# Kernel optimization log

Measured on AMD Instinct MI355X. Metric: run time of the kernel, lower is better.

The kernel has to match this reference:

```python
import jax, jax.numpy as jnp
import numpy as np

TIME_GAP_BUCKETS = 64
B, L, H, MAX_T = 256, 200, 256, 256
VOCAB, N_GROUPS = 50000, 16
EPS = 1e-5


def setup_inputs() -> dict:
    key = jax.random.key(0)
    ks = jax.random.split(key, 16)
    lengths = jax.random.randint(ks[0], (B,), 0, L + 1)
    mask = jnp.arange(L)[None, :] < lengths[:, None]

    def toks(k, hi):  # jagged padded-dense: zeros past each row's length
        return jnp.where(mask, jax.random.randint(k, (B, L), 0, hi), 0)

    inp = {
        'history_tokens': toks(ks[1], VOCAB),
        'history_post_tokens': toks(ks[2], VOCAB),
        'history_author_tokens': toks(ks[3], VOCAB),
        'history_action_tokens': toks(ks[4], VOCAB),
        'history_time_gap': toks(ks[5], TIME_GAP_BUCKETS + 1),
        'history_group_ids': jnp.where(mask, jnp.sort(jax.random.randint(ks[6], (B, L), 1, N_GROUPS + 1), axis=1), 0),
        'lengths': lengths,
    }
    s = 0.02
    inp['token_emb'] = jax.random.normal(ks[7], (VOCAB, H)) * s
    inp['ln_gamma'] = jnp.ones((6 * H,))
    inp['ln_beta'] = jnp.zeros((6 * H,))
    inp['w1'] = jax.random.normal(ks[8], (6 * H, 4 * H)) * (1.0 / np.sqrt(6 * H)).astype(np.float32)
    inp['b1'] = jnp.zeros((4 * H,))
    inp['w2'] = jax.random.normal(ks[9], (4 * H, H)) * (1.0 / np.sqrt(4 * H)).astype(np.float32)
    inp['b2'] = jnp.zeros((H,))
    inp['time_gap_emb'] = (jax.random.normal(ks[10], (TIME_GAP_BUCKETS + 1, H)) * s).at[0].set(0.0)  # padding_idx=0
    inp['group_emb'] = (jax.random.normal(ks[11], (N_GROUPS + 1, H)) * s).at[0].set(0.0)  # padding_idx=0
    inp['pos_emb'] = jax.random.normal(ks[12], (MAX_T, H)) * s
    inp['sep_token'] = jax.random.normal(ks[13], (H,)) * 0.02
    return inp


def _layernorm(x, g, b):
    mu = jnp.mean(x, axis=-1, keepdims=True)
    var = jnp.mean(jnp.square(x - mu), axis=-1, keepdims=True)
    return (x - mu) * jax.lax.rsqrt(var + EPS) * g + b


def _merge_with_sep(event_tokens, group_ids, mask, sep_token):
    # mask is a prefix mask (positions < lengths), so valid tokens are contiguous.
    Bn, Ln, Hn = event_tokens.shape
    next_mask = jnp.pad(mask[:, 1:], ((0, 0), (0, 1)))
    next_group = jnp.pad(group_ids[:, 1:], ((0, 0), (0, 1)))
    sep_after = mask & next_mask & (group_ids != next_group)  # insert sep after token i
    seps_before = jnp.cumsum(sep_after, axis=1) - sep_after.astype(jnp.int32)  # exclusive scan
    token_pos = jnp.arange(Ln)[None, :] + seps_before  # position within merged piece list
    total = mask.sum(axis=1) + sep_after.sum(axis=1)  # [B] merged piece count
    offset = MAX_T - total  # right-align; negative -> leading pieces dropped
    tok_idx = offset[:, None] + token_pos
    sep_idx = tok_idx + 1
    tok_idx = jnp.where(mask & (tok_idx >= 0), tok_idx, MAX_T)  # MAX_T => dropped
    sep_idx = jnp.where(sep_after & (sep_idx >= 0), sep_idx, MAX_T)
    sep_rows = jnp.broadcast_to(sep_token, (Ln, Hn))

    def scatter_one(ev, ti, si):
        buf = jnp.zeros((MAX_T, Hn), ev.dtype)
        buf = buf.at[ti].set(ev, mode='drop')
        buf = buf.at[si].set(sep_rows, mode='drop')
        return buf

    merged = jax.vmap(scatter_one)(event_tokens, tok_idx, sep_idx)
    merged_len = jnp.minimum(total, MAX_T)
    merged_mask = jnp.arange(MAX_T)[None, :] >= (MAX_T - merged_len)[:, None]
    return merged, merged_mask


def reference(history_tokens, history_post_tokens, history_author_tokens,
              history_action_tokens, history_time_gap, history_group_ids,
              lengths, token_emb, ln_gamma, ln_beta, w1, b1, w2, b2,
              time_gap_emb, group_emb, pos_emb, sep_token):
    mask = jnp.arange(L)[None, :] < lengths[:, None]
    hh = token_emb[history_tokens]
    ph = token_emb[history_post_tokens]
    ah = token_emb[history_author_tokens]
    ch = token_emb[history_action_tokens]
    th = time_gap_emb[jnp.clip(history_time_gap, 0, TIME_GAP_BUCKETS)]
    gh = group_emb[history_group_ids]
    ev = jnp.concatenate([hh, ph, ah, ch, th, gh], axis=-1)  # [B, L, 6H]
    x = _layernorm(ev, ln_gamma, ln_beta)
    x = jax.nn.silu(x @ w1 + b1)  # dropout is identity in eval mode
    event_tokens = x @ w2 + b2  # [B, L, H]
    merged, mm = _merge_with_sep(event_tokens, history_group_ids, mask, sep_token)
    merged = (merged + pos_emb[None]) * mm[..., None].astype(merged.dtype)
    return merged, mm
```

## Files before the change

### kernel.cpp

```cpp
#include <hip/hip_runtime.h>
#include <hip/hip_bf16.h>
#include <math.h>

#define B_    256
#define L_    200
#define H_    256
#define MAXT  256
#define SIXH  1536
#define FOURH 1024
#define NPOS  (B_ * L_)

typedef __attribute__((ext_vector_type(8))) short short8;
typedef __attribute__((ext_vector_type(4))) float f32x4;

typedef __attribute__((address_space(3))) void lds_void;
typedef const __attribute__((address_space(1))) void gbl_void;

#define ASM_BAR() asm volatile("s_barrier" ::: "memory")
#define VMCNT4()  asm volatile("s_waitcnt vmcnt(4)" ::: "memory")
#define VMCNT0()  asm volatile("s_waitcnt vmcnt(0)" ::: "memory")

__global__ void scan_offsets(const int* __restrict__ lengths,
                             int* __restrict__ offsets) {
  if (threadIdx.x == 0) {
    int acc = 0;
    for (int b = 0; b < B_; b++) { offsets[b] = acc; acc += lengths[b]; }
    offsets[B_] = acc;
  }
}

__global__ void zero_pad_x(__hip_bfloat16* __restrict__ x,
                           const int* __restrict__ offsets) {
  int total = offsets[B_];
  int padded = (total + 255) & ~255;
  int row = total + blockIdx.x;
  if (row >= padded) return;
  int t = threadIdx.x;
#pragma unroll
  for (int j = 0; j < 6; j++)
    x[(size_t)row * SIXH + j * 256 + t] = __float2bfloat16(0.0f);
}

__global__ void tpos_kernel(const int* __restrict__ gids,
                            const int* __restrict__ lengths,
                            const int* __restrict__ offsets,
                            int* __restrict__ tpos) {
  int b = blockIdx.x, t = threadIdx.x;
  __shared__ int g[L_];
  int len = lengths[b];
  for (int l = t; l < len; l += 64) g[l] = gids[b * L_ + l];
  __syncthreads();
  if (t != 0) return;
  int base = offsets[b];
  int nsep = 0;
  for (int l = 0; l + 1 < len; l++)
    if (g[l] != g[l + 1]) nsep++;
  int total = len + nsep;
  int off = MAXT - total;
  int sb = 0;
  for (int l = 0; l < len; l++) {
    int ti = off + l + sb;
    tpos[base + l] = (ti >= 0) ? (b * MAXT + ti) : -1;
    if (l + 1 < len && g[l] != g[l + 1]) sb++;
  }
}

__global__ void transpose_to_bf16(const float* __restrict__ in,
                                  __hip_bfloat16* __restrict__ out,
                                  int R, int C) {
  __shared__ float tile[32][33];
  int tc = blockIdx.x, tr = blockIdx.y;
  int tx = threadIdx.x & 31, ty = threadIdx.x >> 5;
#pragma unroll
  for (int i = 0; i < 4; i++) {
    int r = tr * 32 + ty + i * 8;
    int c = tc * 32 + tx;
    tile[ty + i * 8][tx] = in[(size_t)r * C + c];
  }
  __syncthreads();
#pragma unroll
  for (int i = 0; i < 4; i++) {
    int orow = tc * 32 + ty + i * 8;
    int ocol = tr * 32 + tx;
    out[(size_t)orow * R + ocol] = __float2bfloat16(tile[tx][ty + i * 8]);
  }
}

__global__ void embed_ln_kernel(const int* __restrict__ tok0,
                                const int* __restrict__ tok1,
                                const int* __restrict__ tok2,
                                const int* __restrict__ tok3,
                                const int* __restrict__ tgap,
                                const int* __restrict__ gid,
                                const int* __restrict__ lengths,
                                const int* __restrict__ offsets,
                                const float* __restrict__ token_emb,
                                const float* __restrict__ tg_emb,
                                const float* __restrict__ g_emb,
                                const float* __restrict__ gamma,
                                const float* __restrict__ beta,
                                __hip_bfloat16* __restrict__ xout) {
  int l = blockIdx.x, b = blockIdx.y;
  if (l >= lengths[b]) return;
  int pos = b * L_ + l;
  int row = offsets[b] + l;
  int t = threadIdx.x;
  int wv = t >> 6;
  int ln = t & 63;
  int c4 = ln * 4;

  const float* tab;
  int idx;
  if (wv == 0)      { tab = token_emb; idx = tok0[pos]; }
  else if (wv == 1) { tab = token_emb; idx = tok1[pos]; }
  else if (wv == 2) { tab = token_emb; idx = tok2[pos]; }
  else if (wv == 3) { tab = token_emb; idx = tok3[pos]; }
  else if (wv == 4) { tab = tg_emb;    idx = min(max(tgap[pos], 0), 64); }
  else              { tab = g_emb;     idx = gid[pos]; }

  float4 v = *(const float4*)&tab[(size_t)idx * H_ + c4];

  float s = v.x + v.y + v.z + v.w;
  float q = v.x * v.x + v.y * v.y + v.z * v.z + v.w * v.w;
#pragma unroll
  for (int o = 32; o; o >>= 1) { s += __shfl_down(s, o); q += __shfl_down(q, o); }
  __shared__ float ps[6], pq[6];
  if (ln == 0) { ps[wv] = s; pq[wv] = q; }
  __syncthreads();
  float ts = 0.f, tq = 0.f;
#pragma unroll
  for (int k = 0; k < 6; k++) { ts += ps[k]; tq += pq[k]; }
  float mu = ts * (1.0f / 1536.0f);
  float var = tq * (1.0f / 1536.0f) - mu * mu;
  float rstd = rsqrtf(var + 1e-5f);

  int cbase = wv * 256 + c4;
  float4 gm = *(const float4*)&gamma[cbase];
  float4 bt = *(const float4*)&beta[cbase];
  float y0 = (v.x - mu) * rstd * gm.x + bt.x;
  float y1 = (v.y - mu) * rstd * gm.y + bt.y;
  float y2 = (v.z - mu) * rstd * gm.z + bt.z;
  float y3 = (v.w - mu) * rstd * gm.w + bt.w;
  __hip_bfloat16 h0 = __float2bfloat16(y0), h1 = __float2bfloat16(y1);
  __hip_bfloat16 h2 = __float2bfloat16(y2), h3 = __float2bfloat16(y3);
  ushort4 pk;
  pk.x = *(unsigned short*)&h0; pk.y = *(unsigned short*)&h1;
  pk.z = *(unsigned short*)&h2; pk.w = *(unsigned short*)&h3;
  *(ushort4*)&xout[(size_t)row * SIXH + cbase] = pk;
}

__global__ __launch_bounds__(512, 2)
void gemm1_8ph(const __hip_bfloat16* __restrict__ A,
               const __hip_bfloat16* __restrict__ Bt,
               const float* __restrict__ bias,
               __hip_bfloat16* __restrict__ out,
               const int* __restrict__ total_ptr) {
  constexpr int K = SIXH;
  constexpr int NT = K / 64;
  constexpr int N = FOURH;

  extern __shared__ __align__(16) char lds[];

  int total = total_ptr[0];
  int padded = (total + 255) & ~255;
  int num_mt = padded >> 8;

  int bid = blockIdx.x;
  int xcd = bid & 7;
  int slot = bid >> 3;
  int nt = slot & 3;
  int mtb = slot >> 2;
  int n0 = nt * 256;

  int tid = threadIdx.x;
  int lane = tid & 63;
  int w = tid >> 6;
  int wave_m = w >> 2;
  int wave_n = w & 3;

  int r15 = lane & 15, g = lane >> 4;
  int slot_r = (((r15 & 1) << 2) | g) ^ (r15 >> 1);
  int lane_off = (r15 >> 1) * 128 + slot_r * 16;

  int s0 = (tid & 7) ^ ((tid >> 3) & 7);
  int scol = (s0 & 3) * 8;
  int row0 = ((tid >> 3) << 1) + (s0 >> 2);
  int ldst0 = w * 1024;

  float bv4[4];
#pragma unroll
  for (int ni = 0; ni < 4; ni++)
    bv4[ni] = bias[n0 + wave_n * 64 + ni * 16 + r15];

#define REGA(d, h) (lds + (d) * 65536 + (h) * 16384)
#define REGB(d, h) (lds + (d) * 65536 + 32768 + (h) * 16384)

#define STAGE(P, t0, kt, h, rb)                                                \
  do {                                                                         \
    __builtin_amdgcn_global_load_lds(                                          \
        (gbl_void*)((P) + (size_t)((t0) + row0) * K + (kt) * 64 + (h) * 32 +   \
                    scol),                                                     \
        (lds_void*)((rb) + ldst0), 16, 0, 0);                                  \
    __builtin_amdgcn_global_load_lds(                                          \
        (gbl_void*)((P) + (size_t)((t0) + row0 + 128) * K + (kt) * 64 +        \
                    (h) * 32 + scol),                                          \
        (lds_void*)((rb) + 8192 + ldst0), 16, 0, 0);                           \
  } while (0)

  for (int mt = xcd + 8 * mtb; mt < num_mt; mt += 64) {
    int m0 = mt * 256;

    f32x4 acc[8][4] = {};

    STAGE(A, m0, 0, 0, REGA(0, 0));
    STAGE(Bt, n0, 0, 0, REGB(0, 0));
    STAGE(A, m0, 0, 1, REGA(0, 1));
    STAGE(Bt, n0, 0, 1, REGB(0, 1));
    STAGE(A, m0, 1, 0, REGA(1, 0));
    STAGE(Bt, n0, 1, 0, REGB(1, 0));
    VMCNT4();
    ASM_BAR();

    for (int kt = 0; kt < NT; ++kt) {
      int d = kt & 1;
      int kc1 = (kt + 1 < NT) ? kt + 1 : NT - 1;
      int kc2 = (kt + 2 < NT) ? kt + 2 : NT - 1;
      char* A0 = REGA(d, 0); char* A1 = REGA(d, 1);
      char* B0 = REGB(d, 0); char* B1 = REGB(d, 1);
      char* An1 = REGA(d ^ 1, 1);
      char* Bn1 = REGB(d ^ 1, 1);

      short8 a[4], b[4];

#pragma unroll
      for (int ni = 0; ni < 4; ni++)
        b[ni] = *(const short8*)(B0 + (wave_n * 64 + ni * 16) * 64 + lane_off);
#pragma unroll
      for (int j = 0; j < 4; j++)
        a[j] = *(const short8*)(A0 + (wave_m * 128 + j * 16) * 64 + lane_off);
      STAGE(A, m0, kc1, 1, An1);
      __builtin_amdgcn_s_setprio(1);
#pragma unroll
      for (int j = 0; j < 4; j++)
#pragma unroll
        for (int ni = 0; ni < 4; ni++)
          acc[j][ni] = __builtin_amdgcn_mfma_f32_16x16x32_bf16(a[j], b[ni],
                                                               acc[j][ni], 0, 0, 0);
      __builtin_amdgcn_s_setprio(0);
#pragma unroll
      for (int j = 0; j < 4; j++)
        a[j] = *(const short8*)(A0 + (wave_m * 128 + (4 + j) * 16) * 64 + lane_off);
      STAGE(Bt, n0, kc1, 1, Bn1);
      __builtin_amdgcn_s_setprio(1);
#pragma unroll
      for (int j = 0; j < 4; j++)
#pragma unroll
        for (int ni = 0; ni < 4; ni++)
          acc[4 + j][ni] = __builtin_amdgcn_mfma_f32_16x16x32_bf16(
              a[j], b[ni], acc[4 + j][ni], 0, 0, 0);
      __builtin_amdgcn_s_setprio(0);
      ASM_BAR();

#pragma unroll
      for (int ni = 0; ni < 4; ni++)
        b[ni] = *(const short8*)(B1 + (wave_n * 64 + ni * 16) * 64 + lane_off);
#pragma unroll
      for (int j = 0; j < 4; j++)
        a[j] = *(const short8*)(A1 + (wave_m * 128 + j * 16) * 64 + lane_off);
      STAGE(A, m0, kc2, 0, A0);
      __builtin_amdgcn_s_setprio(1);
#pragma unroll
      for (int j = 0; j < 4; j++)
#pragma unroll
        for (int ni = 0; ni < 4; ni++)
          acc[j][ni] = __builtin_amdgcn_mfma_f32_16x16x32_bf16(a[j], b[ni],
                                                               acc[j][ni], 0, 0, 0);
      __builtin_amdgcn_s_setprio(0);
#pragma unroll
      for (int j = 0; j < 4; j++)
        a[j] = *(const short8*)(A1 + (wave_m * 128 + (4 + j) * 16) * 64 + lane_off);
      STAGE(Bt, n0, kc2, 0, B0);
      __builtin_amdgcn_s_setprio(1);
#pragma unroll
      for (int j = 0; j < 4; j++)
#pragma unroll
        for (int ni = 0; ni < 4; ni++)
          acc[4 + j][ni] = __builtin_amdgcn_mfma_f32_16x16x32_bf16(
              a[j], b[ni], acc[4 + j][ni], 0, 0, 0);
      __builtin_amdgcn_s_setprio(0);
      VMCNT4();
      ASM_BAR();
    }
    VMCNT0();

    int r0 = g * 4;
#pragma unroll
    for (int mi = 0; mi < 8; mi++)
#pragma unroll
      for (int ni = 0; ni < 4; ni++) {
        int col = n0 + wave_n * 64 + ni * 16 + r15;
        float bv = bv4[ni];
#pragma unroll
        for (int r = 0; r < 4; r++) {
          int row = m0 + wave_m * 128 + mi * 16 + r0 + r;
          float v = acc[mi][ni][r] + bv;
          v = v / (1.0f + __expf(-v));
          out[(size_t)row * N + col] = __float2bfloat16(v);
        }
      }
  }
#undef STAGE
#undef REGA
#undef REGB
}

__global__ void gemm2_scatter(const __hip_bfloat16* __restrict__ A,
                              const __hip_bfloat16* __restrict__ Bt,
                              const float* __restrict__ bias,
                              const int* __restrict__ tpos,
                              const float* __restrict__ pos_emb,
                              float* __restrict__ out,
                              const int* __restrict__ total_ptr,
                              int N, int K) {
  int m0 = blockIdx.y * 128;
  int total = total_ptr[0];
  int padded = (total + 127) & ~127;
  if (m0 >= padded) return;

  __shared__ __hip_bfloat16 As[128 * 64];
  __shared__ __hip_bfloat16 Bs[128 * 64];
  int n0 = blockIdx.x * 128;
  int tid = threadIdx.x;
  int lane = tid & 63, wid = tid >> 6;
  int wm = (wid >> 1) * 64, wn = (wid & 1) * 64;

  int srow = (lane >> 3);
  int scol = (lane & 7) * 8;

  f32x4 acc[4][4] = {};

  for (int k0 = 0; k0 < K; k0 += 64) {
#pragma unroll
    for (int i = 0; i < 4; i++) {
      int c = wid * 4 + i;
      int row = c * 8 + srow;
      __builtin_amdgcn_global_load_lds(
          (gbl_void*)&A[(size_t)(m0 + row) * K + k0 + scol],
          (lds_void*)(As + c * 512), 16, 0, 0);
      __builtin_amdgcn_global_load_lds(
          (gbl_void*)&Bt[(size_t)(n0 + row) * K + k0 + scol],
          (lds_void*)(Bs + c * 512), 16, 0, 0);
    }
    __syncthreads();
#pragma unroll
    for (int kk = 0; kk < 64; kk += 32) {
      short8 a[4], bb[4];
#pragma unroll
      for (int m = 0; m < 4; m++)
        a[m] = *(const short8*)&As[(wm + m * 16 + (lane & 15)) * 64 + kk +
                                   8 * (lane >> 4)];
#pragma unroll
      for (int n = 0; n < 4; n++)
        bb[n] = *(const short8*)&Bs[(wn + n * 16 + (lane & 15)) * 64 + kk +
                                    8 * (lane >> 4)];
#pragma unroll
      for (int m = 0; m < 4; m++)
#pragma unroll
        for (int n = 0; n < 4; n++)
          acc[m][n] = __builtin_amdgcn_mfma_f32_16x16x32_bf16(a[m], bb[n],
                                                              acc[m][n], 0, 0, 0);
    }
    __syncthreads();
  }

  int r0 = (lane >> 4) * 4;
  int cc = lane & 15;
#pragma unroll
  for (int m = 0; m < 4; m++) {
#pragma unroll
    for (int r = 0; r < 4; r++) {
      int row = m0 + wm + m * 16 + r0 + r;
      if (row >= total) continue;
      int pa = tpos[row];
      if (pa < 0) continue;
      int p = pa & (MAXT - 1);
#pragma unroll
      for (int n = 0; n < 4; n++) {
        int col = n0 + wn + n * 16 + cc;
        float v = acc[m][n][r] + bias[col] + pos_emb[p * H_ + col];
        out[(size_t)pa * H_ + col] = v;
      }
    }
  }
}

__global__ void merge2_kernel(const int* __restrict__ gids,
                              const int* __restrict__ lengths,
                              const float* __restrict__ sep_token,
                              const float* __restrict__ pos_emb,
                              float* __restrict__ out) {
  int b = blockIdx.x, t = threadIdx.x;
  __shared__ signed char src[MAXT];
  __shared__ int g[L_];
  __shared__ int sh_total;
  int len = lengths[b];
  src[t] = 0;
  for (int l = t; l < len; l += 256) g[l] = gids[b * L_ + l];
  __syncthreads();
  if (t == 0) {
    int nsep = 0;
    for (int l = 0; l + 1 < len; l++)
      if (g[l] != g[l + 1]) nsep++;
    int total = len + nsep;
    sh_total = total;
    int off = MAXT - total;
    int sb = 0;
    for (int l = 0; l < len; l++) {
      int ti = off + l + sb;
      if (ti >= 0) src[ti] = 2;
      if (l + 1 < len && g[l] != g[l + 1]) {
        if (ti + 1 >= 0) src[ti + 1] = 1;
        sb++;
      }
    }
  }
  __syncthreads();
  int total = sh_total;
  int mlen = min(total, MAXT);

  int q = t >> 6, lane = t & 63, c4 = lane * 4;
  float4 sep4 = *(const float4*)&sep_token[c4];
  float* orow = out + (size_t)b * MAXT * H_;
  for (int p0 = 0; p0 < MAXT; p0 += 4) {
    int p = p0 + q;
    int s = src[p];
    if (s == 2) continue;
    float4 v;
    if (s == 1) {
      float4 pe = *(const float4*)&pos_emb[p * H_ + c4];
      v.x = sep4.x + pe.x; v.y = sep4.y + pe.y;
      v.z = sep4.z + pe.z; v.w = sep4.w + pe.w;
    } else {
      v.x = 0.f; v.y = 0.f; v.z = 0.f; v.w = 0.f;
    }
    *(float4*)&orow[(size_t)p * H_ + c4] = v;
  }
  float* mm = out + (size_t)B_ * MAXT * H_;
  mm[b * MAXT + t] = (t >= MAXT - mlen) ? 1.0f : 0.0f;
}

extern "C" void kernel_launch(void* const* d_in, const int* in_sizes, int n_in,
                              void* d_out, int out_size, void* d_ws,
                              size_t ws_size, hipStream_t stream) {
  const int* tok0 = (const int*)d_in[0];
  const int* tok1 = (const int*)d_in[1];
  const int* tok2 = (const int*)d_in[2];
  const int* tok3 = (const int*)d_in[3];
  const int* tgap = (const int*)d_in[4];
  const int* gid  = (const int*)d_in[5];
  const int* lengths = (const int*)d_in[6];
  const float* token_emb = (const float*)d_in[7];
  const float* gamma = (const float*)d_in[8];
  const float* beta  = (const float*)d_in[9];
  const float* w1 = (const float*)d_in[10];
  const float* b1 = (const float*)d_in[11];
  const float* w2 = (const float*)d_in[12];
  const float* b2 = (const float*)d_in[13];
  const float* tg_emb = (const float*)d_in[14];
  const float* g_emb  = (const float*)d_in[15];
  const float* pos_emb = (const float*)d_in[16];
  const float* sep_tok = (const float*)d_in[17];

  const size_t NEEDED = 265815044;
  if (ws_size < NEEDED) return;

  char* ws = (char*)d_ws;
  __hip_bfloat16* x = (__hip_bfloat16*)ws;
  int* tpos = (int*)ws;
  __hip_bfloat16* h = (__hip_bfloat16*)(ws + 157286400);
  __hip_bfloat16* w1t = (__hip_bfloat16*)(ws + 262144000);
  __hip_bfloat16* w2t = (__hip_bfloat16*)(ws + 265289728);
  int* offsets = (int*)(ws + 265814016);

  scan_offsets<<<1, 64, 0, stream>>>(lengths, offsets);
  zero_pad_x<<<256, 256, 0, stream>>>(x, offsets);

  transpose_to_bf16<<<dim3(1024 / 32, 1536 / 32), 256, 0, stream>>>(w1, w1t,
                                                                    1536, 1024);
  transpose_to_bf16<<<dim3(256 / 32, 1024 / 32), 256, 0, stream>>>(w2, w2t,
                                                                   1024, 256);

  embed_ln_kernel<<<dim3(L_, B_), 384, 0, stream>>>(
      tok0, tok1, tok2, tok3, tgap, gid, lengths, offsets, token_emb, tg_emb,
      g_emb, gamma, beta, x);

  hipFuncSetAttribute((const void*)gemm1_8ph,
                      hipFuncAttributeMaxDynamicSharedMemorySize, 131072);
  gemm1_8ph<<<256, 512, 131072, stream>>>(x, w1t, b1, h, offsets + B_);

  tpos_kernel<<<B_, 64, 0, stream>>>(gid, lengths, offsets, tpos);

  gemm2_scatter<<<dim3(H_ / 128, NPOS / 128), 256, 0, stream>>>(
      h, w2t, b2, tpos, pos_emb, (float*)d_out, offsets + B_, H_, FOURH);

  merge2_kernel<<<B_, 256, 0, stream>>>(gid, lengths, sep_tok, pos_emb,
                                        (float*)d_out);
}
```

Baseline: 254.4 us.

## Rewrite GEMM1 with 256x128 tiles, BK=32 and higher occupancy; parallelize scan and fuse transposes

Measured after the change: 257.2 us. Within noise of the previous version (+1.1%).

```diff
diff --git a/kernel.cpp b/kernel.cpp
--- a/kernel.cpp
+++ b/kernel.cpp
@@ -17,16 +17,30 @@
 typedef const __attribute__((address_space(1))) void gbl_void;
 
 #define ASM_BAR() asm volatile("s_barrier" ::: "memory")
-#define VMCNT4()  asm volatile("s_waitcnt vmcnt(4)" ::: "memory")
+#define VMCNT3()  asm volatile("s_waitcnt vmcnt(3)" ::: "memory")
 #define VMCNT0()  asm volatile("s_waitcnt vmcnt(0)" ::: "memory")
 
 __global__ void scan_offsets(const int* __restrict__ lengths,
                              int* __restrict__ offsets) {
-  if (threadIdx.x == 0) {
-    int acc = 0;
-    for (int b = 0; b < B_; b++) { offsets[b] = acc; acc += lengths[b]; }
-    offsets[B_] = acc;
-  }
+  int t = threadIdx.x;
+  int lane = t & 63, wv = t >> 6;
+  int len = lengths[t];
+  int s = len;
+#pragma unroll
+  for (int o = 1; o < 64; o <<= 1) {
+    int v = __shfl_up(s, o);
+    if (lane >= o) s += v;
+  }
+  __shared__ int wsum[4];
+  if (lane == 63) wsum[wv] = s;
+  __syncthreads();
+  int pre = 0;
+#pragma unroll
+  for (int k = 0; k < 4; k++)
+    if (k < wv) pre += wsum[k];
+  s += pre;
+  offsets[t] = s - len;
+  if (t == 255) offsets[B_] = s;
 }
 
 __global__ void zero_pad_x(__hip_bfloat16* __restrict__ x,
@@ -65,25 +79,28 @@
   }
 }
 
-__global__ void transpose_to_bf16(const float* __restrict__ in,
-                                  __hip_bfloat16* __restrict__ out,
-                                  int R, int C) {
+__global__ void transpose_both(const float* __restrict__ w1,
+                               __hip_bfloat16* __restrict__ w1t,
+                               const float* __restrict__ w2,
+                               __hip_bfloat16* __restrict__ w2t) {
   __shared__ float tile[32][33];
-  int tc = blockIdx.x, tr = blockIdx.y;
+  int id = blockIdx.x;
+  const float* in; __hip_bfloat16* out; int R, C, tc, tr;
+  if (id < 1536) {
+    in = w1; out = w1t; R = 1536; C = 1024; tc = id & 31; tr = id >> 5;
+  } else {
+    int j = id - 1536;
+    in = w2; out = w2t; R = 1024; C = 256; tc = j & 7; tr = j >> 3;
+  }
   int tx = threadIdx.x & 31, ty = threadIdx.x >> 5;
 #pragma unroll
-  for (int i = 0; i < 4; i++) {
-    int r = tr * 32 + ty + i * 8;
-    int c = tc * 32 + tx;
-    tile[ty + i * 8][tx] = in[(size_t)r * C + c];
-  }
-  __syncthreads();
-#pragma unroll
-  for (int i = 0; i < 4; i++) {
-    int orow = tc * 32 + ty + i * 8;
-    int ocol = tr * 32 + tx;
-    out[(size_t)orow * R + ocol] = __float2bfloat16(tile[tx][ty + i * 8]);
-  }
+  for (int i = 0; i < 4; i++)
+    tile[ty + i * 8][tx] = in[(size_t)(tr * 32 + ty + i * 8) * C + tc * 32 + tx];
+  __syncthreads();
+#pragma unroll
+  for (int i = 0; i < 4; i++)
+    out[(size_t)(tc * 32 + ty + i * 8) * R + tr * 32 + tx] =
+        __float2bfloat16(tile[tx][ty + i * 8]);
 }
 
 __global__ void embed_ln_kernel(const int* __restrict__ tok0,
@@ -149,34 +166,36 @@
   *(ushort4*)&xout[(size_t)row * SIXH + cbase] = pk;
 }
 
-__global__ __launch_bounds__(512, 2)
-void gemm1_8ph(const __hip_bfloat16* __restrict__ A,
-               const __hip_bfloat16* __restrict__ Bt,
-               const float* __restrict__ bias,
-               __hip_bfloat16* __restrict__ out,
-               const int* __restrict__ total_ptr) {
+__global__ __launch_bounds__(512, 4)
+void gemm1_bk32(const __hip_bfloat16* __restrict__ A,
+                const __hip_bfloat16* __restrict__ Bt,
+                const float* __restrict__ bias,
+                __hip_bfloat16* __restrict__ out,
+                const int* __restrict__ total_ptr) {
   constexpr int K = SIXH;
-  constexpr int NT = K / 64;
+  constexpr int NS = K / 32;
   constexpr int N = FOURH;
 
-  extern __shared__ __align__(16) char lds[];
+  __shared__ __align__(16) char lds[49152];
 
   int total = total_ptr[0];
   int padded = (total + 255) & ~255;
   int num_mt = padded >> 8;
 
-  int bid = blockIdx.x;
-  int xcd = bid & 7;
-  int slot = bid >> 3;
-  int nt = slot & 3;
-  int mtb = slot >> 2;
-  int n0 = nt * 256;
+  int flat = blockIdx.y * 8 + blockIdx.x;
+  int xcd = flat & 7;
+  int j = flat >> 3;
+  int nt = j & 7;
+  int mt = (j >> 3) * 8 + xcd;
+  if (mt >= num_mt) return;
+  int m0 = mt * 256;
+  int n0 = nt * 128;
 
   int tid = threadIdx.x;
   int lane = tid & 63;
   int w = tid >> 6;
-  int wave_m = w >> 2;
-  int wave_n = w & 3;
+  int wave_m = w >> 1;
+  int wave_n = w & 1;
 
   int r15 = lane & 15, g = lane >> 4;
   int slot_r = (((r15 & 1) << 2) | g) ^ (r15 >> 1);
@@ -185,133 +204,95 @@
   int s0 = (tid & 7) ^ ((tid >> 3) & 7);
   int scol = (s0 & 3) * 8;
   int row0 = ((tid >> 3) << 1) + (s0 >> 2);
-  int ldst0 = w * 1024;
 
   float bv4[4];
 #pragma unroll
   for (int ni = 0; ni < 4; ni++)
     bv4[ni] = bias[n0 + wave_n * 64 + ni * 16 + r15];
 
-#define REGA(d, h) (lds + (d) * 65536 + (h) * 16384)
-#define REGB(d, h) (lds + (d) * 65536 + 32768 + (h) * 16384)
-
-#define STAGE(P, t0, kt, h, rb)                                                \
+#define AREG(d) (lds + (d) * 16384)
+#define BREG(d) (lds + 32768 + (d) * 8192)
+
+#define STAGE_A(ks, d)                                                         \
   do {                                                                         \
     __builtin_amdgcn_global_load_lds(                                          \
-        (gbl_void*)((P) + (size_t)((t0) + row0) * K + (kt) * 64 + (h) * 32 +   \
-                    scol),                                                     \
-        (lds_void*)((rb) + ldst0), 16, 0, 0);                                  \
+        (gbl_void*)(A + (size_t)(m0 + row0) * K + (ks) * 32 + scol),           \
+        (lds_void*)(AREG(d) + (size_t)tid * 16 % 8192 + 0 * 8192 +             \
+                    (tid * 16 / 8192) * 0),                                    \
+        16, 0, 0);                                                             \
+  } while (0)
+#undef STAGE_A
+#define STAGE_A(ks, d)                                                         \
+  do {                                                                         \
     __builtin_amdgcn_global_load_lds(                                          \
-        (gbl_void*)((P) + (size_t)((t0) + row0 + 128) * K + (kt) * 64 +        \
-                    (h) * 32 + scol),                                          \
-        (lds_void*)((rb) + 8192 + ldst0), 16, 0, 0);                           \
+        (gbl_void*)(A + (size_t)(m0 + row0) * K + (ks) * 32 + scol),           \
+        (lds_void*)(AREG(d) + w * 1024), 16, 0, 0);                            \
+    __builtin_amdgcn_global_load_lds(                                          \
+        (gbl_void*)(A + (size_t)(m0 + row0 + 128) * K + (ks) * 32 + scol),     \
+        (lds_void*)(AREG(d) + 8192 + w * 1024), 16, 0, 0);                     \
   } while (0)
-
-  for (int mt = xcd + 8 * mtb; mt < num_mt; mt += 64) {
-    int m0 = mt * 256;
-
-    f32x4 acc[8][4] = {};
-
-    STAGE(A, m0, 0, 0, REGA(0, 0));
-    STAGE(Bt, n0, 0, 0, REGB(0, 0));
-    STAGE(A, m0, 0, 1, REGA(0, 1));
-    STAGE(Bt, n0, 0, 1, REGB(0, 1));
-    STAGE(A, m0, 1, 0, REGA(1, 0));
-    STAGE(Bt, n0, 1, 0, REGB(1, 0));
-    VMCNT4();
+#define STAGE_B(ks, d)                                                         \
+  __builtin_amdgcn_global_load_lds(                                            \
+      (gbl_void*)(Bt + (size_t)(n0 + row0) * K + (ks) * 32 + scol),            \
+      (lds_void*)(BREG(d) + w * 1024), 16, 0, 0)
+
+  f32x4 acc[4][4] = {};
+
+  STAGE_A(0, 0); STAGE_B(0, 0);
+  STAGE_A(1, 1); STAGE_B(1, 1);
+  VMCNT3();
+  ASM_BAR();
+
+  for (int ks = 0; ks < NS; ++ks) {
+    int d = ks & 1;
+    int kn = (ks + 2 < NS) ? ks + 2 : NS - 1;
+    char* Ad = AREG(d);
+    char* Bd = BREG(d);
+
+    short8 a[4], b[4];
+#pragma unroll
+    for (int ni = 0; ni < 4; ni++)
+      b[ni] = *(const short8*)(Bd + (wave_n * 64 + ni * 16) * 64 + lane_off);
+#pragma unroll
+    for (int mi = 0; mi < 4; mi++)
+      a[mi] = *(const short8*)(Ad + (wave_m * 64 + mi * 16) * 64 + lane_off);
     ASM_BAR();
 
-    for (int kt = 0; kt < NT; ++kt) {
-      int d = kt & 1;
-      int kc1 = (kt + 1 < NT) ? kt + 1 : NT - 1;
-      int kc2 = (kt + 2 < NT) ? kt + 2 : NT - 1;
-      char* A0 = REGA(d, 0); char* A1 = REGA(d, 1);
-      char* B0 = REGB(d, 0); char* B1 = REGB(d, 1);
-      char* An1 = REGA(d ^ 1, 1);
-      char* Bn1 = REGB(d ^ 1, 1);
-
-      short8 a[4], b[4];
-
+    STAGE_A(kn, d); STAGE_B(kn, d);
+
+    __builtin_amdgcn_s_setprio(1);
+#pragma unroll
+    for (int mi = 0; mi < 4; mi++)
 #pragma unroll
       for (int ni = 0; ni < 4; ni++)
-        b[ni] = *(const short8*)(B0 + (wave_n * 64 + ni * 16) * 64 + lane_off);
-#pragma unroll
-      for (int j = 0; j < 4; j++)
-        a[j] = *(const short8*)(A0 + (wave_m * 128 + j * 16) * 64 + lane_off);
-      STAGE(A, m0, kc1, 1, An1);
-      __builtin_amdgcn_s_setprio(1);
-#pragma unroll
-      for (int j = 0; j < 4; j++)
-#pragma unroll
-        for (int ni = 0; ni < 4; ni++)
-          acc[j][ni] = __builtin_amdgcn_mfma_f32_16x16x32_bf16(a[j], b[ni],
-                                                               acc[j][ni], 0, 0, 0);
-      __builtin_amdgcn_s_setprio(0);
-#pragma unroll
-      for (int j = 0; j < 4; j++)
-        a[j] = *(const short8*)(A0 + (wave_m * 128 + (4 + j) * 16) * 64 + lane_off);
-      STAGE(Bt, n0, kc1, 1, Bn1);
-      __builtin_amdgcn_s_setprio(1);
-#pragma unroll
-      for (int j = 0; j < 4; j++)
-#pragma unroll
-        for (int ni = 0; ni < 4; ni++)
-          acc[4 + j][ni] = __builtin_amdgcn_mfma_f32_16x16x32_bf16(
-              a[j], b[ni], acc[4 + j][ni], 0, 0, 0);
-      __builtin_amdgcn_s_setprio(0);
-      ASM_BAR();
-
-#pragma unroll
-      for (int ni = 0; ni < 4; ni++)
-        b[ni] = *(const short8*)(B1 + (wave_n * 64 + ni * 16) * 64 + lane_off);
-#pragma unroll
-      for (int j = 0; j < 4; j++)
-        a[j] = *(const short8*)(A1 + (wave_m * 128 + j * 16) * 64 + lane_off);
-      STAGE(A, m0, kc2, 0, A0);
-      __builtin_amdgcn_s_setprio(1);
-#pragma unroll
-      for (int j = 0; j < 4; j++)
-#pragma unroll
-        for (int ni = 0; ni < 4; ni++)
-          acc[j][ni] = __builtin_amdgcn_mfma_f32_16x16x32_bf16(a[j], b[ni],
-                                                               acc[j][ni], 0, 0, 0);
-      __builtin_amdgcn_s_setprio(0);
-#pragma unroll
-      for (int j = 0; j < 4; j++)
-        a[j] = *(const short8*)(A1 + (wave_m * 128 + (4 + j) * 16) * 64 + lane_off);
-      STAGE(Bt, n0, kc2, 0, B0);
-      __builtin_amdgcn_s_setprio(1);
-#pragma unroll
-      for (int j = 0; j < 4; j++)
-#pragma unroll
-        for (int ni = 0; ni < 4; ni++)
-          acc[4 + j][ni] = __builtin_amdgcn_mfma_f32_16x16x32_bf16(
-              a[j], b[ni], acc[4 + j][ni], 0, 0, 0);
-      __builtin_amdgcn_s_setprio(0);
-      VMCNT4();
-      ASM_BAR();
-    }
-    VMCNT0();
-
-    int r0 = g * 4;
-#pragma unroll
-    for (int mi = 0; mi < 8; mi++)
-#pragma unroll
-      for (int ni = 0; ni < 4; ni++) {
-        int col = n0 + wave_n * 64 + ni * 16 + r15;
-        float bv = bv4[ni];
-#pragma unroll
-        for (int r = 0; r < 4; r++) {
-          int row = m0 + wave_m * 128 + mi * 16 + r0 + r;
-          float v = acc[mi][ni][r] + bv;
-          v = v / (1.0f + __expf(-v));
-          out[(size_t)row * N + col] = __float2bfloat16(v);
-        }
+        acc[mi][ni] = __builtin_amdgcn_mfma_f32_16x16x32_bf16(a[mi], b[ni],
+                                                              acc[mi][ni], 0, 0, 0);
+    __builtin_amdgcn_s_setprio(0);
+
+    VMCNT3();
+    ASM_BAR();
+  }
+  VMCNT0();
+
+  int r0 = g * 4;
+#pragma unroll
+  for (int mi = 0; mi < 4; mi++)
+#pragma unroll
+    for (int ni = 0; ni < 4; ni++) {
+      int col = n0 + wave_n * 64 + ni * 16 + r15;
+      float bv = bv4[ni];
+#pragma unroll
+      for (int r = 0; r < 4; r++) {
+        int row = m0 + wave_m * 64 + mi * 16 + r0 + r;
+        float v = acc[mi][ni][r] + bv;
+        v = v / (1.0f + __expf(-v));
+        out[(size_t)row * N + col] = __float2bfloat16(v);
       }
-  }
-#undef STAGE
-#undef REGA
-#undef REGB
+    }
+#undef STAGE_A
+#undef STAGE_B
+#undef AREG
+#undef BREG
 }
 
 __global__ void gemm2_scatter(const __hip_bfloat16* __restrict__ A,
@@ -482,21 +463,17 @@
   __hip_bfloat16* w2t = (__hip_bfloat16*)(ws + 265289728);
   int* offsets = (int*)(ws + 265814016);
 
-  scan_offsets<<<1, 64, 0, stream>>>(lengths, offsets);
+  scan_offsets<<<1, 256, 0, stream>>>(lengths, offsets);
   zero_pad_x<<<256, 256, 0, stream>>>(x, offsets);
 
-  transpose_to_bf16<<<dim3(1024 / 32, 1536 / 32), 256, 0, stream>>>(w1, w1t,
-                                                                    1536, 1024);
-  transpose_to_bf16<<<dim3(256 / 32, 1024 / 32), 256, 0, stream>>>(w2, w2t,
-                                                                   1024, 256);
+  transpose_both<<<1792, 256, 0, stream>>>(w1, w1t, w2, w2t);
 
   embed_ln_kernel<<<dim3(L_, B_), 384, 0, stream>>>(
       tok0, tok1, tok2, tok3, tgap, gid, lengths, offsets, token_emb, tg_emb,
       g_emb, gamma, beta, x);
 
-  hipFuncSetAttribute((const void*)gemm1_8ph,
-                      hipFuncAttributeMaxDynamicSharedMemorySize, 131072);
-  gemm1_8ph<<<256, 512, 131072, stream>>>(x, w1t, b1, h, offsets + B_);
+  gemm1_bk32<<<dim3(8, NPOS / 256), 512, 0, stream>>>(x, w1t, b1, h,
+                                                      offsets + B_);
 
   tpos_kernel<<<B_, 64, 0, stream>>>(gid, lengths, offsets, tpos);
 
```
